# Optimization experiments

Hardware: AMD Instinct MI355X
Metric: run time of the kernel (lower is better)

Reference implementation:

```python
import jax, jax.numpy as jnp
import numpy as np

DIM, H, KVH = 1024, 16, 4
HD = DIM // H            # head_dim = 64
KV_DIM = KVH * HD        # 256
ROPE_BASE = 10000.0
EPS = 1e-6


def setup_inputs() -> dict:
    key = jax.random.key(0)
    ks = jax.random.split(key, 6)
    B, S = 4, 2048
    x = jax.random.normal(ks[0], (B, S, DIM), dtype=jnp.float32)
    sc = 0.02
    Wq = jax.random.normal(ks[1], (DIM, DIM), dtype=jnp.float32) * sc
    Wk = jax.random.normal(ks[2], (KV_DIM, DIM), dtype=jnp.float32) * sc
    Wv = jax.random.normal(ks[3], (KV_DIM, DIM), dtype=jnp.float32) * sc
    Wo = jax.random.normal(ks[4], (DIM, DIM), dtype=jnp.float32) * sc
    q_gain = jnp.full((H,), 1.5, dtype=jnp.float32)
    return {"x": x, "Wq": Wq, "Wk": Wk, "Wv": Wv, "Wo": Wo, "q_gain": q_gain}


def _rms_norm(t):
    return t * jax.lax.rsqrt(jnp.mean(t * t, axis=-1, keepdims=True) + EPS)


def _rotary(seqlen, dtype):
    inv_freq = 1.0 / (ROPE_BASE ** (jnp.arange(0, HD, 2, dtype=jnp.float32) / HD))
    t = jnp.arange(seqlen, dtype=jnp.float32)
    freqs = jnp.outer(t, inv_freq)                      # [S, HD/2]
    return jnp.cos(freqs).astype(dtype)[None, None], jnp.sin(freqs).astype(dtype)[None, None]


def _apply_rot(t, cos, sin):
    half = t.shape[-1] // 2
    t1, t2 = t[..., :half], t[..., half:]
    return jnp.concatenate((t1 * cos + t2 * sin, -t1 * sin + t2 * cos), axis=-1)


def reference(x, Wq, Wk, Wv, Wo, q_gain):
    B, S, D = x.shape
    q = (x @ Wq.T).reshape(B, S, H, HD).transpose(0, 2, 1, 3)      # [B,H,S,HD]
    k = (x @ Wk.T).reshape(B, S, KVH, HD).transpose(0, 2, 1, 3)    # [B,KVH,S,HD]
    v = (x @ Wv.T).reshape(B, S, KVH, HD).transpose(0, 2, 1, 3)
    q, k = _rms_norm(q), _rms_norm(k)
    cos, sin = _rotary(S, q.dtype)
    q, k = _apply_rot(q, cos, sin), _apply_rot(k, cos, sin)
    q = q * q_gain.astype(q.dtype)[None, :, None, None]
    rep = H // KVH
    k_exp = jnp.repeat(k, rep, axis=1)                              # GQA expand
    v_exp = jnp.repeat(v, rep, axis=1)
    scores = jnp.einsum('bhqd,bhkd->bhqk', q, k_exp) / np.sqrt(HD)
    causal = jnp.tril(jnp.ones((S, S), dtype=bool))
    scores = jnp.where(causal[None, None], scores, jnp.finfo(scores.dtype).min)
    attn = jax.nn.softmax(scores, axis=-1)
    y = jnp.einsum('bhqk,bhkd->bhqd', attn, v_exp)
    y = y.transpose(0, 2, 1, 3).reshape(B, S, D)
    return y @ Wo.T
```

## Files before the change

### kernel.cpp

```cpp
#include <hip/hip_runtime.h>

typedef float f32x4 __attribute__((ext_vector_type(4)));
typedef float f32x16 __attribute__((ext_vector_type(16)));
typedef __bf16 bf16x8 __attribute__((ext_vector_type(8)));
typedef unsigned short u16x8 __attribute__((ext_vector_type(8)));
typedef int i32x2 __attribute__((ext_vector_type(2)));
typedef int i32x4 __attribute__((ext_vector_type(4)));

#define DEV static __device__ __forceinline__

DEV float bf2f(unsigned short h) {
  unsigned int u = ((unsigned int)h) << 16;
  return __builtin_bit_cast(float, u);
}
DEV unsigned short f2bf(float f) {
  unsigned int u = __builtin_bit_cast(unsigned int, f);
  u += 0x7fff + ((u >> 16) & 1);
  return (unsigned short)(u >> 16);
}

DEV void g2l16(const void* g, void* l) {
  __builtin_amdgcn_global_load_lds(
      (const __attribute__((address_space(1))) void*)g,
      (__attribute__((address_space(3))) void*)l, 16, 0, 0);
}

DEV unsigned int cvtpk(float lo, float hi) {
  unsigned int r;
  asm("v_cvt_pk_bf16_f32 %0, %1, %2" : "=v"(r) : "v"(lo), "v"(hi));
  return r;
}

DEV void cvt8(const float* __restrict__ in, unsigned short* __restrict__ out, int idx) {
  int i = idx * 8;
  float4 a = *(const float4*)(in + i);
  float4 b = *(const float4*)(in + i + 4);
  u16x8 r;
  r[0] = f2bf(a.x); r[1] = f2bf(a.y); r[2] = f2bf(a.z); r[3] = f2bf(a.w);
  r[4] = f2bf(b.x); r[5] = f2bf(b.y); r[6] = f2bf(b.z); r[7] = f2bf(b.w);
  *(u16x8*)(out + i) = r;
}

__global__ __launch_bounds__(256) void k_cvt_all(const float* __restrict__ x,
                                                 const float* __restrict__ wq,
                                                 const float* __restrict__ wk,
                                                 const float* __restrict__ wv,
                                                 const float* __restrict__ wo,
                                                 unsigned short* __restrict__ xb,
                                                 unsigned short* __restrict__ wcat,
                                                 unsigned short* __restrict__ wob,
                                                 float2* __restrict__ rope) {
  const int blk = blockIdx.x, tid = threadIdx.x;
  if (blk < 4096) {
    cvt8(x, xb, blk * 256 + tid);
  } else if (blk < 4608) {
    cvt8(wq, wcat, (blk - 4096) * 256 + tid);
  } else if (blk < 4736) {
    cvt8(wk, wcat + 1048576, (blk - 4608) * 256 + tid);
  } else if (blk < 4864) {
    cvt8(wv, wcat + 1310720, (blk - 4736) * 256 + tid);
  } else if (blk < 5376) {
    cvt8(wo, wob, (blk - 4864) * 256 + tid);
  } else {
    int idx = (blk - 5376) * 256 + tid;
    int s = idx >> 5, dmod = idx & 31;
    float inv_freq = powf(10000.0f, -(float)dmod * (1.0f / 32.0f));
    float sn, cs;
    sincosf((float)s * inv_freq, &sn, &cs);
    rope[idx] = make_float2(cs, sn);
  }
}

__global__ __launch_bounds__(256) void k_qkv(const unsigned short* __restrict__ A,
                                             const unsigned short* __restrict__ B,
                                             const float* __restrict__ qg,
                                             const float2* __restrict__ rope,
                                             unsigned short* __restrict__ qn,
                                             unsigned short* __restrict__ kn,
                                             unsigned short* __restrict__ vt) {
  __shared__ unsigned short LDS[16384];
  unsigned short* As = LDS;
  unsigned short* Bs = LDS + 8192;
  const int K = 1024;
  const int tid = threadIdx.x;
  const int wid = tid >> 6, lane = tid & 63;
  const int g = lane >> 4, r16 = lane & 15;
  const int m0 = blockIdx.x * 128;
  const int y = blockIdx.y;
  const int n0 = y * 128;
  const int wr = wid >> 1, wc = wid & 1;

  f32x4 acc[4][4];
#pragma unroll
  for (int i = 0; i < 4; ++i)
#pragma unroll
    for (int j = 0; j < 4; ++j) acc[i][j] = f32x4{0.f, 0.f, 0.f, 0.f};

  const int cb = (lane & 7) * 16;

  for (int k0 = 0; k0 < K; k0 += 64) {
#pragma unroll
    for (int c = 0; c < 4; ++c) {
      int i = wid * 4 + c;
      int row = i * 8 + (lane >> 3);
      int sc = cb ^ ((row & 7) << 4);
      g2l16((const char*)A + ((size_t)(m0 + row) * K + k0) * 2 + sc, (char*)As + i * 1024);
      g2l16((const char*)B + ((size_t)(n0 + row) * K + k0) * 2 + sc, (char*)Bs + i * 1024);
    }
    __syncthreads();
#pragma unroll
    for (int kh = 0; kh < 2; ++kh) {
      bf16x8 af[4], bfr[4];
#pragma unroll
      for (int m = 0; m < 4; ++m) {
        int row = wr * 64 + m * 16 + r16;
        int byte = row * 128 + ((g * 16 + kh * 64) ^ ((row & 7) << 4));
        af[m] = *(const bf16x8*)((const char*)As + byte);
      }
#pragma unroll
      for (int n = 0; n < 4; ++n) {
        int row = wc * 64 + n * 16 + r16;
        int byte = row * 128 + ((g * 16 + kh * 64) ^ ((row & 7) << 4));
        bfr[n] = *(const bf16x8*)((const char*)Bs + byte);
      }
#pragma unroll
      for (int m = 0; m < 4; ++m)
#pragma unroll
        for (int n = 0; n < 4; ++n)
          acc[m][n] = __builtin_amdgcn_mfma_f32_16x16x32_bf16(af[m], bfr[n], acc[m][n], 0, 0, 0);
    }
    __syncthreads();
  }

  if (y < 10) {
    const bool isq = (y < 8);
    const int head = isq ? (2 * y + wc) : (2 * (y - 8) + wc);
    const float gain = isq ? qg[head] * 0.18033688011112042f : 1.0f;
#pragma unroll
    for (int m = 0; m < 4; ++m)
#pragma unroll
      for (int j = 0; j < 4; ++j) {
        int rowl = wr * 64 + m * 16 + g * 4 + j;
        int tok = m0 + rowl;
        int s = tok & 2047;
        float v0 = acc[m][0][j], v1 = acc[m][1][j], v2 = acc[m][2][j], v3 = acc[m][3][j];
        float ss = v0 * v0 + v1 * v1 + v2 * v2 + v3 * v3;
        ss += __shfl_xor(ss, 1); ss += __shfl_xor(ss, 2);
        ss += __shfl_xor(ss, 4); ss += __shfl_xor(ss, 8);
        float rs = rsqrtf(ss * (1.0f / 64.0f) + 1e-6f) * gain;
        float2 cs0 = rope[s * 32 + r16];
        float2 cs1 = rope[s * 32 + 16 + r16];
        float o0 = (v0 * cs0.x + v2 * cs0.y) * rs;
        float o2 = (v2 * cs0.x - v0 * cs0.y) * rs;
        float o1 = (v1 * cs1.x + v3 * cs1.y) * rs;
        float o3 = (v3 * cs1.x - v1 * cs1.y) * rs;
        unsigned short* dst = isq ? (qn + (size_t)tok * 1024 + head * 64)
                                  : (kn + (size_t)tok * 256 + head * 64);
        dst[r16] = f2bf(o0);
        dst[16 + r16] = f2bf(o1);
        dst[32 + r16] = f2bf(o2);
        dst[48 + r16] = f2bf(o3);
      }
  } else {
    unsigned short* T = LDS;
#pragma unroll
    for (int m = 0; m < 4; ++m)
#pragma unroll
      for (int n = 0; n < 4; ++n)
#pragma unroll
        for (int j = 0; j < 4; ++j) {
          int tokl = wr * 64 + m * 16 + g * 4 + j;
          int dl = wc * 64 + n * 16 + r16;
          int byte = (dl * 256 + tokl * 2) ^ ((dl & 15) << 4);
          *(unsigned short*)((char*)T + byte) = f2bf(acc[m][n][j]);
        }
    __syncthreads();
    const int d = tid >> 1, th = tid & 1;
    const int hv = 2 * (y - 10) + (d >> 6), dh = d & 63;
    const int bb = m0 >> 11;
    const int s0 = (m0 & 2047) + th * 64;
    unsigned short* dstv = vt + ((size_t)(bb * 4 + hv) * 64 + dh) * 2048 + s0;
    const int swz = (d & 15) << 4;
#pragma unroll
    for (int c = 0; c < 8; ++c) {
      i32x4 w = *(const i32x4*)((const char*)T + ((d * 256 + th * 128 + c * 16) ^ swz));
      *(i32x4*)(dstv + c * 8) = w;
    }
  }
}

__global__ __launch_bounds__(256) void k_gemm_bt(const unsigned short* __restrict__ A,
                                                 const unsigned short* __restrict__ B,
                                                 float* __restrict__ C, int M, int N, int K) {
  __shared__ unsigned short As[128 * 64];
  __shared__ unsigned short Bs[128 * 64];
  const int tid = threadIdx.x;
  const int wid = tid >> 6, lane = tid & 63;
  const int g = lane >> 4, r16 = lane & 15;
  const int m0 = blockIdx.x * 128, n0 = blockIdx.y * 128;
  const int wr = wid >> 1, wc = wid & 1;

  f32x4 acc[4][4];
#pragma unroll
  for (int i = 0; i < 4; ++i)
#pragma unroll
    for (int j = 0; j < 4; ++j) acc[i][j] = f32x4{0.f, 0.f, 0.f, 0.f};

  const int cb = (lane & 7) * 16;

  for (int k0 = 0; k0 < K; k0 += 64) {
#pragma unroll
    for (int c = 0; c < 4; ++c) {
      int i = wid * 4 + c;
      int row = i * 8 + (lane >> 3);
      int sc = cb ^ ((row & 7) << 4);
      g2l16((const char*)A + ((size_t)(m0 + row) * K + k0) * 2 + sc, (char*)As + i * 1024);
      g2l16((const char*)B + ((size_t)(n0 + row) * K + k0) * 2 + sc, (char*)Bs + i * 1024);
    }
    __syncthreads();
#pragma unroll
    for (int kh = 0; kh < 2; ++kh) {
      bf16x8 af[4], bfr[4];
#pragma unroll
      for (int m = 0; m < 4; ++m) {
        int row = wr * 64 + m * 16 + r16;
        int byte = row * 128 + ((g * 16 + kh * 64) ^ ((row & 7) << 4));
        af[m] = *(const bf16x8*)((const char*)As + byte);
      }
#pragma unroll
      for (int n = 0; n < 4; ++n) {
        int row = wc * 64 + n * 16 + r16;
        int byte = row * 128 + ((g * 16 + kh * 64) ^ ((row & 7) << 4));
        bfr[n] = *(const bf16x8*)((const char*)Bs + byte);
      }
#pragma unroll
      for (int m = 0; m < 4; ++m)
#pragma unroll
        for (int n = 0; n < 4; ++n)
          acc[m][n] = __builtin_amdgcn_mfma_f32_16x16x32_bf16(af[m], bfr[n], acc[m][n], 0, 0, 0);
    }
    __syncthreads();
  }
#pragma unroll
  for (int m = 0; m < 4; ++m)
#pragma unroll
    for (int n = 0; n < 4; ++n)
#pragma unroll
      for (int j = 0; j < 4; ++j) {
        int row = m0 + wr * 64 + m * 16 + g * 4 + j;
        int col = n0 + wc * 64 + n * 16 + r16;
        C[(size_t)row * N + col] = acc[m][n][j];
      }
}

__global__ __launch_bounds__(256) void k_attn2(const unsigned short* __restrict__ qn,
                                               const unsigned short* __restrict__ kn,
                                               const unsigned short* __restrict__ vt,
                                               unsigned short* __restrict__ yb) {
  __shared__ unsigned short SMEM[4 * 8192];
  const int tid = threadIdx.x;
  const int wid = tid >> 6, lane = tid & 63;
  const int hi = lane >> 5, l31 = lane & 31;
  const int flat = blockIdx.x;
  const int qx = 15 - (flat >> 6);
  const int bh = flat & 63;
  const int b = bh >> 4, h = bh & 15, hv = h >> 2;
  const int q0w = qx * 128 + wid * 32;
  const int qglob = q0w + l31;
  const size_t tok0 = (size_t)b * 2048;
  const unsigned short* vtb = vt + (size_t)(b * 4 + hv) * 64 * 2048;

  const u16x8 onesu = {0x3F80, 0x3F80, 0x3F80, 0x3F80, 0x3F80, 0x3F80, 0x3F80, 0x3F80};
  const bf16x8 ones = __builtin_bit_cast(bf16x8, onesu);

  bf16x8 qf[4];
#pragma unroll
  for (int m = 0; m < 4; ++m)
    qf[m] = *(const bf16x8*)(qn + (tok0 + qglob) * 1024 + h * 64 + m * 16 + hi * 8);

  f32x16 oacc[2], lacc, zer;
#pragma unroll
  for (int r = 0; r < 16; ++r) { oacc[0][r] = 0.f; oacc[1][r] = 0.f; lacc[r] = 0.f; zer[r] = 0.f; }

  auto stage = [&](int T, int tb) {
    unsigned short* KsB = SMEM + tb * 8192;
    unsigned short* VtB = KsB + 4096;
    const int kk0 = T * 64;
#pragma unroll
    for (int c = 0; c < 2; ++c) {
      int i = wid * 2 + c;
      int row = i * 8 + (lane >> 3);
      int sc = ((lane & 7) * 16) ^ ((row & 7) << 4);
      g2l16((const char*)(kn + (tok0 + kk0 + row) * 256 + hv * 64) + sc, (char*)KsB + i * 1024);
      g2l16((const char*)(vtb + (size_t)row * 2048 + kk0) + sc, (char*)VtB + i * 1024);
    }
  };

  auto qk_tile = [&](int tb, f32x16* s) {
    const char* kbase0 = (const char*)SMEM + tb * 16384;
#pragma unroll
    for (int kt = 0; kt < 2; ++kt) {
      const int krow = kt * 32 + l31;
      const char* kbase = kbase0 + krow * 128;
      const int ksw = (krow & 7) << 4;
      __builtin_amdgcn_s_setprio(1);
      bf16x8 kf = *(const bf16x8*)(kbase + ((hi * 16) ^ ksw));
      f32x16 a = __builtin_amdgcn_mfma_f32_32x32x16_bf16(kf, qf[0], zer, 0, 0, 0);
#pragma unroll
      for (int m = 1; m < 4; ++m) {
        kf = *(const bf16x8*)(kbase + ((m * 32 + hi * 16) ^ ksw));
        a = __builtin_amdgcn_mfma_f32_32x32x16_bf16(kf, qf[m], a, 0, 0, 0);
      }
      __builtin_amdgcn_s_setprio(0);
      s[kt] = a;
    }
  };

  auto mask_tile = [&](int t, f32x16* s) {
    const int k0 = t * 64;
#pragma unroll
    for (int kt = 0; kt < 2; ++kt)
#pragma unroll
      for (int r = 0; r < 16; ++r) {
        int key = k0 + kt * 32 + (r & 3) + 8 * (r >> 2) + 4 * hi;
        if (key > qglob) s[kt][r] = -INFINITY;
      }
  };

  auto softmax_cvt = [&](f32x16* s, i32x4* paw) {
#pragma unroll
    for (int kt = 0; kt < 2; ++kt)
#pragma unroll
      for (int r = 0; r < 16; ++r) s[kt][r] = exp2f(s[kt][r]);
#pragma unroll
    for (int kt = 0; kt < 2; ++kt)
#pragma unroll
      for (int half = 0; half < 2; ++half) {
        int bs = half * 8;
        unsigned int a0 = cvtpk(s[kt][bs + 0], s[kt][bs + 1]);
        unsigned int a1 = cvtpk(s[kt][bs + 2], s[kt][bs + 3]);
        unsigned int b0 = cvtpk(s[kt][bs + 4], s[kt][bs + 5]);
        unsigned int b1 = cvtpk(s[kt][bs + 6], s[kt][bs + 7]);
        i32x2 r0 = __builtin_amdgcn_permlane32_swap((int)a0, (int)b0, false, false);
        i32x2 r1 = __builtin_amdgcn_permlane32_swap((int)a1, (int)b1, false, false);
        i32x4 w;
        w[0] = r0[0]; w[1] = r1[0]; w[2] = r0[1]; w[3] = r1[1];
        paw[kt * 2 + half] = w;
      }
  };

  auto pv_tile = [&](int tb, const i32x4* paw) {
    const char* vbase0 = (const char*)SMEM + tb * 16384 + 8192;
    __builtin_amdgcn_s_setprio(1);
#pragma unroll
    for (int db = 0; db < 2; ++db) {
      const int vrow = db * 32 + l31;
      const char* vbase = vbase0 + vrow * 128;
      const int vsw = (vrow & 7) << 4;
#pragma unroll
      for (int ks = 0; ks < 4; ++ks) {
        bf16x8 vf = *(const bf16x8*)(vbase + ((ks * 32 + hi * 16) ^ vsw));
        oacc[db] = __builtin_amdgcn_mfma_f32_32x32x16_bf16(
            vf, __builtin_bit_cast(bf16x8, paw[ks]), oacc[db], 0, 0, 0);
      }
    }
#pragma unroll
    for (int ks = 0; ks < 4; ++ks)
      lacc = __builtin_amdgcn_mfma_f32_32x32x16_bf16(
          ones, __builtin_bit_cast(bf16x8, paw[ks]), lacc, 0, 0, 0);
    __builtin_amdgcn_s_setprio(0);
  };

  const int npair = qx + 1;

  stage(0, 0);
  stage(1, 1);
  __syncthreads();

  for (int p = 0; p < npair - 1; ++p) {
    const int pb = (p & 1) << 1;
    const int nb = pb ^ 2;
    stage(2 * p + 2, nb);
    stage(2 * p + 3, nb | 1);
    f32x16 sa[2], sb[2];
    qk_tile(pb, sa);
    qk_tile(pb | 1, sb);
    i32x4 pawa[4], pawb[4];
    softmax_cvt(sa, pawa);
    pv_tile(pb, pawa);
    softmax_cvt(sb, pawb);
    pv_tile(pb | 1, pawb);
    __syncthreads();
  }
  {
    const int p = npair - 1;
    const int pb = (p & 1) << 1;
    const int t0 = 2 * p;
    f32x16 sa[2], sb[2];
    qk_tile(pb, sa);
    qk_tile(pb | 1, sb);
    mask_tile(t0, sa);
    mask_tile(t0 + 1, sb);
    i32x4 pawa[4], pawb[4];
    softmax_cvt(sa, pawa);
    pv_tile(pb, pawa);
    softmax_cvt(sb, pawb);
    pv_tile(pb | 1, pawb);
    __syncthreads();
  }

  const float inv = 1.0f / lacc[0];
  const int swl = (l31 & 7) << 4;
  char* obase = (char*)SMEM + wid * 4096;
#pragma unroll
  for (int db = 0; db < 2; ++db)
#pragma unroll
    for (int i = 0; i < 8; ++i) {
      int r = 2 * i;
      int dim = db * 32 + (r & 3) + 8 * (r >> 2) + 4 * hi;
      unsigned int w = (unsigned int)f2bf(oacc[db][r] * inv) |
                       ((unsigned int)f2bf(oacc[db][r + 1] * inv) << 16);
      *(unsigned int*)(obase + l31 * 128 + ((dim * 2) ^ swl)) = w;
    }
  __syncthreads();
#pragma unroll
  for (int it = 0; it < 4; ++it) {
    int cc = it * 2 + hi;
    i32x4 w = *(const i32x4*)(obase + l31 * 128 + ((cc * 16) ^ swl));
    *(i32x4*)(yb + (tok0 + q0w + l31) * 1024 + h * 64 + cc * 8) = w;
  }
}

extern "C" void kernel_launch(void* const* d_in, const int* in_sizes, int n_in,
                              void* d_out, int out_size, void* d_ws, size_t ws_size,
                              hipStream_t stream) {
  (void)in_sizes; (void)n_in; (void)out_size; (void)ws_size;
  const float* x  = (const float*)d_in[0];
  const float* Wq = (const float*)d_in[1];
  const float* Wk = (const float*)d_in[2];
  const float* Wv = (const float*)d_in[3];
  const float* Wo = (const float*)d_in[4];
  const float* qg = (const float*)d_in[5];

  char* ws = (char*)d_ws;
  unsigned short* xb   = (unsigned short*)(ws);
  unsigned short* wcat = (unsigned short*)(ws + 16777216);
  unsigned short* wob  = (unsigned short*)(ws + 19922944);
  unsigned short* qn   = (unsigned short*)(ws + 22020096);
  unsigned short* kn   = (unsigned short*)(ws + 38797312);
  unsigned short* yb   = xb;
  unsigned short* vt   = (unsigned short*)((char*)d_out + 25165824);
  float2*         rope = (float2*)((char*)d_out + 29360128);

  k_cvt_all<<<5632, 256, 0, stream>>>(x, Wq, Wk, Wv, Wo, xb, wcat, wob, rope);
  k_qkv<<<dim3(64, 12), 256, 0, stream>>>(xb, wcat, qg, rope, qn, kn, vt);
  k_attn2<<<1024, 256, 0, stream>>>(qn, kn, vt, yb);
  k_gemm_bt<<<dim3(64, 8), 256, 0, stream>>>(yb, wob, (float*)d_out, 8192, 1024, 1024);
}
```

Before: 151.9 us.

## Widen attention blocks to eight waves with per-wave causal tile skipping

The attention kernel now launches 512-thread blocks that each cover 256 query rows, so each staged K/V tile is shared by twice as many waves. This halves the global K/V traffic per query and the number of staging instructions per thread. The loop is unified: each wave skips QK/softmax/PV work on tiles entirely above its own causal diagonal, and masks only in the last two pairs. exp2f is replaced with raw v_exp_f32 to drop the libm wrapper. The risks are fewer blocks (512), which can worsen load balance across CUs on a causal workload, idle waves inside blocks near the diagonal, and higher register pressure at the 512-thread launch bound.

```diff
diff --git a/kernel.cpp b/kernel.cpp
--- a/kernel.cpp
+++ b/kernel.cpp
@@ -28,6 +28,12 @@
 DEV unsigned int cvtpk(float lo, float hi) {
   unsigned int r;
   asm("v_cvt_pk_bf16_f32 %0, %1, %2" : "=v"(r) : "v"(lo), "v"(hi));
+  return r;
+}
+
+DEV float fexp2(float x) {
+  float r;
+  asm("v_exp_f32 %0, %1" : "=v"(r) : "v"(x));
   return r;
 }
 
@@ -253,7 +259,7 @@
       }
 }
 
-__global__ __launch_bounds__(256) void k_attn2(const unsigned short* __restrict__ qn,
+__global__ __launch_bounds__(512) void k_attn2(const unsigned short* __restrict__ qn,
                                                const unsigned short* __restrict__ kn,
                                                const unsigned short* __restrict__ vt,
                                                unsigned short* __restrict__ yb) {
@@ -262,11 +268,12 @@
   const int wid = tid >> 6, lane = tid & 63;
   const int hi = lane >> 5, l31 = lane & 31;
   const int flat = blockIdx.x;
-  const int qx = 15 - (flat >> 6);
+  const int qcx = 7 - (flat >> 6);
   const int bh = flat & 63;
   const int b = bh >> 4, h = bh & 15, hv = h >> 2;
-  const int q0w = qx * 128 + wid * 32;
+  const int q0w = qcx * 256 + wid * 32;
   const int qglob = q0w + l31;
+  const int tdiag = (q0w + 31) >> 6;
   const size_t tok0 = (size_t)b * 2048;
   const unsigned short* vtb = vt + (size_t)(b * 4 + hv) * 64 * 2048;
 
@@ -286,14 +293,10 @@
     unsigned short* KsB = SMEM + tb * 8192;
     unsigned short* VtB = KsB + 4096;
     const int kk0 = T * 64;
-#pragma unroll
-    for (int c = 0; c < 2; ++c) {
-      int i = wid * 2 + c;
-      int row = i * 8 + (lane >> 3);
-      int sc = ((lane & 7) * 16) ^ ((row & 7) << 4);
-      g2l16((const char*)(kn + (tok0 + kk0 + row) * 256 + hv * 64) + sc, (char*)KsB + i * 1024);
-      g2l16((const char*)(vtb + (size_t)row * 2048 + kk0) + sc, (char*)VtB + i * 1024);
-    }
+    int row = wid * 8 + (lane >> 3);
+    int sc = ((lane & 7) * 16) ^ ((row & 7) << 4);
+    g2l16((const char*)(kn + (tok0 + kk0 + row) * 256 + hv * 64) + sc, (char*)KsB + wid * 1024);
+    g2l16((const char*)(vtb + (size_t)row * 2048 + kk0) + sc, (char*)VtB + wid * 1024);
   };
 
   auto qk_tile = [&](int tb, f32x16* s) {
@@ -331,7 +334,7 @@
 #pragma unroll
     for (int kt = 0; kt < 2; ++kt)
 #pragma unroll
-      for (int r = 0; r < 16; ++r) s[kt][r] = exp2f(s[kt][r]);
+      for (int r = 0; r < 16; ++r) s[kt][r] = fexp2(s[kt][r]);
 #pragma unroll
     for (int kt = 0; kt < 2; ++kt)
 #pragma unroll
@@ -371,41 +374,37 @@
     __builtin_amdgcn_s_setprio(0);
   };
 
-  const int npair = qx + 1;
+  const int npair = 2 * qcx + 2;
 
   stage(0, 0);
   stage(1, 1);
   __syncthreads();
 
-  for (int p = 0; p < npair - 1; ++p) {
+  for (int p = 0; p < npair; ++p) {
     const int pb = (p & 1) << 1;
-    const int nb = pb ^ 2;
-    stage(2 * p + 2, nb);
-    stage(2 * p + 3, nb | 1);
+    if (p + 1 < npair) {
+      stage(2 * p + 2, pb ^ 2);
+      stage(2 * p + 3, (pb ^ 2) | 1);
+    }
+    const int t0 = 2 * p;
+    const bool visa = (t0 <= tdiag), visb = (t0 + 1 <= tdiag);
+    const bool domask = (p >= npair - 2);
     f32x16 sa[2], sb[2];
-    qk_tile(pb, sa);
-    qk_tile(pb | 1, sb);
+    if (visa) qk_tile(pb, sa);
+    if (visb) qk_tile(pb | 1, sb);
+    if (domask) {
+      if (visa) mask_tile(t0, sa);
+      if (visb) mask_tile(t0 + 1, sb);
+    }
     i32x4 pawa[4], pawb[4];
-    softmax_cvt(sa, pawa);
-    pv_tile(pb, pawa);
-    softmax_cvt(sb, pawb);
-    pv_tile(pb | 1, pawb);
-    __syncthreads();
-  }
-  {
-    const int p = npair - 1;
-    const int pb = (p & 1) << 1;
-    const int t0 = 2 * p;
-    f32x16 sa[2], sb[2];
-    qk_tile(pb, sa);
-    qk_tile(pb | 1, sb);
-    mask_tile(t0, sa);
-    mask_tile(t0 + 1, sb);
-    i32x4 pawa[4], pawb[4];
-    softmax_cvt(sa, pawa);
-    pv_tile(pb, pawa);
-    softmax_cvt(sb, pawb);
-    pv_tile(pb | 1, pawb);
+    if (visa) {
+      softmax_cvt(sa, pawa);
+      pv_tile(pb, pawa);
+    }
+    if (visb) {
+      softmax_cvt(sb, pawb);
+      pv_tile(pb | 1, pawb);
+    }
     __syncthreads();
   }
 
@@ -454,6 +453,6 @@
 
   k_cvt_all<<<5632, 256, 0, stream>>>(x, Wq, Wk, Wv, Wo, xb, wcat, wob, rope);
   k_qkv<<<dim3(64, 12), 256, 0, stream>>>(xb, wcat, qg, rope, qn, kn, vt);
-  k_attn2<<<1024, 256, 0, stream>>>(qn, kn, vt, yb);
+  k_attn2<<<512, 512, 0, stream>>>(qn, kn, vt, yb);
   k_gemm_bt<<<dim3(64, 8), 256, 0, stream>>>(yb, wob, (float*)d_out, 8192, 1024, 1024);
 }
```

Measured after the change: 134.2 us. 1.13x faster.
